# Kernel optimization log

Measured on AMD Instinct MI355X. Metric: run time of the kernel, lower is better.

The kernel has to match this reference:

```python
import jax, jax.numpy as jnp
import numpy as np

VOCAB = 100000
HIDDEN = 128
BATCH = 1024
LEN = 200


def setup_inputs() -> dict:
    key = jax.random.key(0)
    k_ids, k_w, k_b = jax.random.split(key, 3)
    word_ids = jax.random.randint(k_ids, (BATCH, LEN), 0, VOCAB)
    # nn.Linear(vocab_sz, hidden_sz): weight [hidden, vocab], bias [hidden]
    bound = 1.0 / np.sqrt(VOCAB)
    W = jax.random.uniform(k_w, (HIDDEN, VOCAB), jnp.float32, -bound, bound)
    b = jax.random.uniform(k_b, (HIDDEN,), jnp.float32, -bound, bound)
    return {"word_ids": word_ids, "W": W, "b": b}


def reference(word_ids, W, b):
    B, L = word_ids.shape
    # bag-of-words histogram: count occurrences of each word per scene
    rows = jnp.broadcast_to(jnp.arange(B)[:, None], (B, L))  # [B, L]
    hist = jnp.zeros((B, W.shape[1]), dtype=W.dtype).at[rows, word_ids].add(1.0)
    # dense linear: y = hist @ W^T + b
    return jnp.einsum("bv,hv->bh", hist, W) + b
```

## Files before the change

### kernel.cpp

```cpp
#include <hip/hip_runtime.h>

#define VOCAB 100000
#define HIDDEN 128
#define BATCH 1024
#define LEN 200

__global__ __launch_bounds__(256) void wt_transpose_kernel(
    const float* __restrict__ W, float* __restrict__ WT) {
    __shared__ float tile[32][133];
    const int v0 = blockIdx.x * 128;
    const int h0 = blockIdx.y * 32;
    const int tid = threadIdx.x;

    const int vx = tid & 31;
    const int hy = tid >> 5;
#pragma unroll
    for (int i = 0; i < 4; ++i) {
        const int h = hy + i * 8;
        const int gv = v0 + vx * 4;
        if (gv + 3 < VOCAB) {
            const float4 f = *reinterpret_cast<const float4*>(
                &W[(size_t)(h0 + h) * VOCAB + gv]);
            tile[h][vx * 4 + 0] = f.x;
            tile[h][vx * 4 + 1] = f.y;
            tile[h][vx * 4 + 2] = f.z;
            tile[h][vx * 4 + 3] = f.w;
        } else {
#pragma unroll
            for (int k = 0; k < 4; ++k)
                if (gv + k < VOCAB)
                    tile[h][vx * 4 + k] = W[(size_t)(h0 + h) * VOCAB + gv + k];
        }
    }
    __syncthreads();

    const int hx = tid & 31;
    const int vy = tid >> 5;
#pragma unroll
    for (int i = 0; i < 16; ++i) {
        const int v = vy + i * 8;
        const int gv = v0 + v;
        if (gv < VOCAB)
            WT[(size_t)gv * HIDDEN + h0 + hx] = tile[hx][v];
    }
}

__global__ __launch_bounds__(512) void bag_gather_kernel(
    const int* __restrict__ ids, const float* __restrict__ WT,
    const float* __restrict__ bias, float* __restrict__ out) {
    __shared__ int sid[LEN];
    __shared__ float4 part[16][32];

    const int b = blockIdx.x;
    const int tid = threadIdx.x;

    for (int l = tid; l < LEN; l += 512) sid[l] = ids[b * LEN + l];
    __syncthreads();

    const int hq = tid & 31;
    const int chunk = tid >> 5;
    const float4* __restrict__ WT4 = reinterpret_cast<const float4*>(WT);

    float4 acc = make_float4(0.f, 0.f, 0.f, 0.f);
    for (int l = chunk; l < LEN; l += 16) {
        const int id = sid[l];
        const float4 w = WT4[(size_t)id * (HIDDEN / 4) + hq];
        acc.x += w.x; acc.y += w.y; acc.z += w.z; acc.w += w.w;
    }
    part[chunk][hq] = acc;
    __syncthreads();

#pragma unroll
    for (int s = 8; s > 0; s >>= 1) {
        if (chunk < s) {
            const float4 o = part[chunk + s][hq];
            float4 m = part[chunk][hq];
            m.x += o.x; m.y += o.y; m.z += o.z; m.w += o.w;
            part[chunk][hq] = m;
        }
        __syncthreads();
    }

    if (chunk == 0) {
        float4 r = part[0][hq];
        const float4 bb = reinterpret_cast<const float4*>(bias)[hq];
        r.x += bb.x; r.y += bb.y; r.z += bb.z; r.w += bb.w;
        reinterpret_cast<float4*>(out)[(size_t)b * (HIDDEN / 4) + hq] = r;
    }
}

__global__ __launch_bounds__(HIDDEN) void bag_direct_kernel(
    const int* __restrict__ ids, const float* __restrict__ W,
    const float* __restrict__ bias, float* __restrict__ out) {
    __shared__ int sid[LEN];
    const int b = blockIdx.x;
    const int h = threadIdx.x;
    for (int l = h; l < LEN; l += HIDDEN) sid[l] = ids[b * LEN + l];
    __syncthreads();
    float acc = 0.f;
    for (int l = 0; l < LEN; ++l)
        acc += W[(size_t)h * VOCAB + sid[l]];
    out[(size_t)b * HIDDEN + h] = acc + bias[h];
}

extern "C" void kernel_launch(void* const* d_in, const int* in_sizes, int n_in,
                              void* d_out, int out_size, void* d_ws, size_t ws_size,
                              hipStream_t stream) {
    const int*   ids  = (const int*)d_in[0];
    const float* W    = (const float*)d_in[1];
    const float* bias = (const float*)d_in[2];
    float*       out  = (float*)d_out;

    const size_t need = (size_t)VOCAB * HIDDEN * sizeof(float);
    if (ws_size >= need) {
        float* WT = (float*)d_ws;
        wt_transpose_kernel<<<dim3((VOCAB + 127) / 128, HIDDEN / 32), 256, 0, stream>>>(W, WT);
        bag_gather_kernel<<<BATCH, 512, 0, stream>>>(ids, WT, bias, out);
    } else {
        bag_direct_kernel<<<BATCH, HIDDEN, 0, stream>>>(ids, W, bias, out);
    }
}
```

Before: 110.0 us.

## Store transposed weight table in fp16 and gather halves with shuffle reduction

The transpose kernel now writes W^T as fp16 instead of fp32, using nontemporal loads and a full-hidden 64-row tile per block. This halves both the write traffic of the transpose and the gather traffic of the bag-sum kernel. The gather kernel reads 16-byte rows of 8 halves per thread, accumulates in fp32, and reduces across chunks with wave shuffles plus a small shared-memory pass instead of a tree of syncthreads. The cost is lower precision from rounding the weights to fp16, which may exceed the allowed tolerance for small-magnitude weights.

```diff
diff --git a/kernel.cpp b/kernel.cpp
--- a/kernel.cpp
+++ b/kernel.cpp
@@ -1,91 +1,107 @@
 #include <hip/hip_runtime.h>
+#include <hip/hip_fp16.h>
 
 #define VOCAB 100000
 #define HIDDEN 128
 #define BATCH 1024
 #define LEN 200
+#define TP_V 64
 
-__global__ __launch_bounds__(256) void wt_transpose_kernel(
-    const float* __restrict__ W, float* __restrict__ WT) {
-    __shared__ float tile[32][133];
-    const int v0 = blockIdx.x * 128;
-    const int h0 = blockIdx.y * 32;
-    const int tid = threadIdx.x;
+typedef float f32x4 __attribute__((ext_vector_type(4)));
 
-    const int vx = tid & 31;
-    const int hy = tid >> 5;
+__global__ __launch_bounds__(256) void wt_transpose_f16(
+    const float* __restrict__ W, __half* __restrict__ WT) {
+    __shared__ float tile[TP_V][133];
+    const int v0 = blockIdx.x * TP_V;
+    const int t  = threadIdx.x;
+
+    const int vx = t & 15;
+    const int hy = t >> 4;
 #pragma unroll
-    for (int i = 0; i < 4; ++i) {
-        const int h = hy + i * 8;
+    for (int p = 0; p < 8; ++p) {
+        const int h  = hy + p * 16;
         const int gv = v0 + vx * 4;
+        f32x4 f;
         if (gv + 3 < VOCAB) {
-            const float4 f = *reinterpret_cast<const float4*>(
-                &W[(size_t)(h0 + h) * VOCAB + gv]);
-            tile[h][vx * 4 + 0] = f.x;
-            tile[h][vx * 4 + 1] = f.y;
-            tile[h][vx * 4 + 2] = f.z;
-            tile[h][vx * 4 + 3] = f.w;
+            f = __builtin_nontemporal_load(
+                reinterpret_cast<const f32x4*>(&W[(size_t)h * VOCAB + gv]));
         } else {
-#pragma unroll
-            for (int k = 0; k < 4; ++k)
-                if (gv + k < VOCAB)
-                    tile[h][vx * 4 + k] = W[(size_t)(h0 + h) * VOCAB + gv + k];
+            f[0] = (gv + 0 < VOCAB) ? W[(size_t)h * VOCAB + gv + 0] : 0.f;
+            f[1] = (gv + 1 < VOCAB) ? W[(size_t)h * VOCAB + gv + 1] : 0.f;
+            f[2] = (gv + 2 < VOCAB) ? W[(size_t)h * VOCAB + gv + 2] : 0.f;
+            f[3] = (gv + 3 < VOCAB) ? W[(size_t)h * VOCAB + gv + 3] : 0.f;
         }
+        tile[vx * 4 + 0][h] = f[0];
+        tile[vx * 4 + 1][h] = f[1];
+        tile[vx * 4 + 2][h] = f[2];
+        tile[vx * 4 + 3][h] = f[3];
     }
     __syncthreads();
 
-    const int hx = tid & 31;
-    const int vy = tid >> 5;
+    const int h8 = (t & 15) * 8;
 #pragma unroll
-    for (int i = 0; i < 16; ++i) {
-        const int v = vy + i * 8;
+    for (int p = 0; p < 4; ++p) {
+        const int v  = (t >> 4) + p * 16;
         const int gv = v0 + v;
-        if (gv < VOCAB)
-            WT[(size_t)gv * HIDDEN + h0 + hx] = tile[hx][v];
+        if (gv < VOCAB) {
+            __half hb[8];
+#pragma unroll
+            for (int k = 0; k < 8; ++k) hb[k] = __float2half_rn(tile[v][h8 + k]);
+            *reinterpret_cast<float4*>(&WT[(size_t)gv * HIDDEN + h8]) =
+                *reinterpret_cast<const float4*>(hb);
+        }
     }
 }
 
-__global__ __launch_bounds__(512) void bag_gather_kernel(
-    const int* __restrict__ ids, const float* __restrict__ WT,
+__global__ __launch_bounds__(512) void bag_gather_f16(
+    const int* __restrict__ ids, const __half* __restrict__ WT,
     const float* __restrict__ bias, float* __restrict__ out) {
-    __shared__ int sid[LEN];
-    __shared__ float4 part[16][32];
+    __shared__ int   sid[LEN];
+    __shared__ float part[8][HIDDEN];
 
     const int b = blockIdx.x;
-    const int tid = threadIdx.x;
+    const int t = threadIdx.x;
 
-    for (int l = tid; l < LEN; l += 512) sid[l] = ids[b * LEN + l];
+    for (int l = t; l < LEN; l += 512) sid[l] = ids[b * LEN + l];
     __syncthreads();
 
-    const int hq = tid & 31;
-    const int chunk = tid >> 5;
-    const float4* __restrict__ WT4 = reinterpret_cast<const float4*>(WT);
+    const int g     = t & 15;
+    const int chunk = t >> 4;
 
-    float4 acc = make_float4(0.f, 0.f, 0.f, 0.f);
-    for (int l = chunk; l < LEN; l += 16) {
+    float acc[8];
+#pragma unroll
+    for (int k = 0; k < 8; ++k) acc[k] = 0.f;
+
+    for (int l = chunk; l < LEN; l += 32) {
         const int id = sid[l];
-        const float4 w = WT4[(size_t)id * (HIDDEN / 4) + hq];
-        acc.x += w.x; acc.y += w.y; acc.z += w.z; acc.w += w.w;
+        const float4 q = *reinterpret_cast<const float4*>(
+            WT + (size_t)id * HIDDEN + g * 8);
+        const __half2* h2 = reinterpret_cast<const __half2*>(&q);
+#pragma unroll
+        for (int k = 0; k < 4; ++k) {
+            const float2 f = __half22float2(h2[k]);
+            acc[2 * k + 0] += f.x;
+            acc[2 * k + 1] += f.y;
+        }
     }
-    part[chunk][hq] = acc;
+
+#pragma unroll
+    for (int k = 0; k < 8; ++k) {
+        acc[k] += __shfl_xor(acc[k], 16);
+        acc[k] += __shfl_xor(acc[k], 32);
+    }
+    const int wave = t >> 6;
+    if ((t & 63) < 16) {
+#pragma unroll
+        for (int k = 0; k < 8; ++k) part[wave][g * 8 + k] = acc[k];
+    }
     __syncthreads();
 
+    if (t < HIDDEN) {
+        float s = 0.f;
 #pragma unroll
-    for (int s = 8; s > 0; s >>= 1) {
-        if (chunk < s) {
-            const float4 o = part[chunk + s][hq];
-            float4 m = part[chunk][hq];
-            m.x += o.x; m.y += o.y; m.z += o.z; m.w += o.w;
-            part[chunk][hq] = m;
-        }
-        __syncthreads();
-    }
-
-    if (chunk == 0) {
-        float4 r = part[0][hq];
-        const float4 bb = reinterpret_cast<const float4*>(bias)[hq];
-        r.x += bb.x; r.y += bb.y; r.z += bb.z; r.w += bb.w;
-        reinterpret_cast<float4*>(out)[(size_t)b * (HIDDEN / 4) + hq] = r;
+        for (int w = 0; w < 8; ++w) s += part[w][t];
+        out[(size_t)b * HIDDEN + t] = s + bias[t];
     }
 }
 
@@ -111,11 +127,11 @@
     const float* bias = (const float*)d_in[2];
     float*       out  = (float*)d_out;
 
-    const size_t need = (size_t)VOCAB * HIDDEN * sizeof(float);
+    const size_t need = (size_t)VOCAB * HIDDEN * sizeof(__half);
     if (ws_size >= need) {
-        float* WT = (float*)d_ws;
-        wt_transpose_kernel<<<dim3((VOCAB + 127) / 128, HIDDEN / 32), 256, 0, stream>>>(W, WT);
-        bag_gather_kernel<<<BATCH, 512, 0, stream>>>(ids, WT, bias, out);
+        __half* WT = (__half*)d_ws;
+        wt_transpose_f16<<<(VOCAB + TP_V - 1) / TP_V, 256, 0, stream>>>(W, WT);
+        bag_gather_f16<<<BATCH, 512, 0, stream>>>(ids, WT, bias, out);
     } else {
         bag_direct_kernel<<<BATCH, HIDDEN, 0, stream>>>(ids, W, bias, out);
     }
```

Result: no change. 108.9 us (-1.0%).
